# Kernel optimization log

Hardware: AMD Instinct MI355X
Metric: run time of the kernel (lower is better)

## Reference

```python
import jax, jax.numpy as jnp
import numpy as np

N = 262144        # 64^3 grid unknowns
NNZ = 7 * N       # ~7-point stencil sparsity
BS = 32


def setup_inputs() -> dict:
    key = jax.random.key(0)
    k1, k2, k3, k4, k5 = jax.random.split(key, 5)
    y_pred = jax.random.normal(k1, (BS, N), dtype=jnp.float32)
    y_true = jax.random.normal(k2, (BS, N), dtype=jnp.float32)
    A_vals = jax.random.normal(k3, (NNZ,), dtype=jnp.float32)
    A_rows = jax.random.randint(k4, (NNZ,), 0, N, dtype=jnp.int32)
    A_cols = jax.random.randint(k5, (NNZ,), 0, N, dtype=jnp.int32)
    return {"y_pred": y_pred, "y_true": y_true, "A_vals": A_vals,
            "A_rows": A_rows, "A_cols": A_cols}


def reference(y_pred, y_true, A_vals, A_rows, A_cols):
    # YhatY[b] = <y_true[b], y_pred[b]>
    YhatY = jnp.sum(y_true * y_pred, axis=1)                      # (bs,)
    # Sparse matvec per batch: YhatAt = (A @ y_pred.T).T, COO form.
    # gathered[e, b] = A_vals[e] * y_pred[b, A_cols[e]]
    gathered = (y_pred[:, A_cols] * A_vals).T                     # (nnz, bs)
    YhatAt = jax.ops.segment_sum(gathered, A_rows, num_segments=N).T  # (bs, N)
    # YhatYhatAt[b] = <y_pred[b], A y_pred[b]>
    YhatYhatAt = jnp.sum(y_pred * YhatAt, axis=1)                 # (bs,)
    # diag(YhatY / YhatYhatAt) @ YhatAt == row-wise scale by alpha
    alpha = YhatY / YhatYhatAt                                    # (bs,)
    resid = y_true - alpha[:, None] * YhatAt                      # (bs, N)
    return jnp.mean(jnp.sum(resid * resid, axis=1))
```

## Files before the change

### kernel.cpp

```cpp
#include <hip/hip_runtime.h>

#define NGRID 262144
#define NNZ_C 1835008
#define TP    260


__global__ __launch_bounds__(256) void k_prep(
        const float* __restrict__ yp, const float* __restrict__ yt,
        float* __restrict__ yp_t, float* __restrict__ yat_t,
        float* __restrict__ p1) {
    __shared__ __align__(16) float T[32 * TP];
    __shared__ float p1red[32];
    const int tid = threadIdx.x;
    const int l = tid & 63, w = tid >> 6;
    const size_t n0 = (size_t)blockIdx.x * 256;
    #pragma unroll
    for (int s = 0; s < 8; ++s) {
        const int b = s * 4 + w;
        const float4 a = *(const float4*)(yp + (size_t)b * NGRID + n0 + 4 * l);
        const float4 t = *(const float4*)(yt + (size_t)b * NGRID + n0 + 4 * l);
        *(float4*)(&T[b * TP + 4 * l]) = a;
        float sty = a.x * t.x + a.y * t.y + a.z * t.z + a.w * t.w;
        #pragma unroll
        for (int o = 32; o > 0; o >>= 1) sty += __shfl_down(sty, o);
        if (l == 0) p1red[b] = sty;
    }
    __syncthreads();
    float4* ypt4 = (float4*)(yp_t + n0 * 32);
    float4* yat4 = (float4*)(yat_t + n0 * 32);
    #pragma unroll
    for (int q = 0; q < 8; ++q) {
        const int f = q * 256 + tid;
        const int n = f >> 3;
        const int bb = 4 * (f & 7);
        float4 v;
        v.x = T[(bb + 0) * TP + n];
        v.y = T[(bb + 1) * TP + n];
        v.z = T[(bb + 2) * TP + n];
        v.w = T[(bb + 3) * TP + n];
        ypt4[f] = v;
        yat4[f] = make_float4(0.f, 0.f, 0.f, 0.f);
    }
    if (tid < 32) p1[blockIdx.x * 32 + tid] = p1red[tid];
}

__global__ void k_scatter(const float* __restrict__ vals,
                          const int* __restrict__ rows,
                          const int* __restrict__ cols,
                          const float* __restrict__ yp_t,
                          float* __restrict__ yat_t) {
    const size_t tid = (size_t)blockIdx.x * blockDim.x + threadIdx.x;
    const int b = (int)(tid & 31);
    const size_t e = tid >> 5;
    const float v = vals[e];
    const int r = rows[e];
    const int c = cols[e];
    const float x = yp_t[(size_t)c * 32 + b];
    atomicAdd(&yat_t[(size_t)r * 32 + b], v * x);
}

__global__ __launch_bounds__(256) void k_post(
        const float* __restrict__ yat_t, const float* __restrict__ yp_t,
        const float* __restrict__ yt, float* __restrict__ p2) {
    __shared__ float tile[256 * 33];
    __shared__ float red[2][256];
    const int tid = threadIdx.x;
    const size_t n0 = (size_t)blockIdx.x * 256;

    float c1 = 0.f, c3 = 0.f;
    #pragma unroll
    for (int i = 0; i < 32; ++i) {
        const int f = i * 256 + tid;
        const float a = yat_t[n0 * 32 + f];
        const float p = yp_t[n0 * 32 + f];
        c1 = fmaf(p, a, c1);
        c3 = fmaf(a, a, c3);
        tile[(f >> 5) * 33 + (f & 31)] = a;
    }
    red[0][tid] = c1;
    red[1][tid] = c3;
    __syncthreads();

    const int w = tid >> 6;
    const int lane = tid & 63;
    #pragma unroll
    for (int j = 0; j < 8; ++j) {
        const int b = w * 8 + j;
        const float* ytr = yt + (size_t)b * NGRID + n0;
        float c2 = 0.f, tt = 0.f;
        #pragma unroll
        for (int c = 0; c < 4; ++c) {
            const int nl = c * 64 + lane;
            const float t = ytr[nl];
            const float yv = tile[nl * 33 + b];
            c2 = fmaf(t, yv, c2);
            tt = fmaf(t, t, tt);
        }
        #pragma unroll
        for (int o = 32; o > 0; o >>= 1) {
            c2 += __shfl_down(c2, o);
            tt += __shfl_down(tt, o);
        }
        if (lane == 0) {
            p2[blockIdx.x * 128 + 32 + b] = c2;
            p2[blockIdx.x * 128 + 96 + b] = tt;
        }
    }

    if (tid < 32) {
        float s1 = 0.f, s3 = 0.f;
        #pragma unroll
        for (int k = 0; k < 8; ++k) {
            s1 += red[0][tid + 32 * k];
            s3 += red[1][tid + 32 * k];
        }
        p2[blockIdx.x * 128 + 0 + tid] = s1;
        p2[blockIdx.x * 128 + 64 + tid] = s3;
    }
}

__global__ __launch_bounds__(256) void k_finish(
        const float* __restrict__ p2, const float* __restrict__ p1,
        float* __restrict__ out) {
    __shared__ float tot[128];
    __shared__ float styv[32];
    __shared__ float lb[32];
    const int tid = threadIdx.x;
    if (tid < 128) {
        float acc = 0.f;
        for (int j = 0; j < 1024; ++j) acc += p2[(size_t)j * 128 + tid];
        tot[tid] = acc;
    } else if (tid < 160) {
        const int b = tid - 128;
        float acc = 0.f;
        for (int j = 0; j < 1024; ++j) acc += p1[(size_t)j * 32 + b];
        styv[b] = acc;
    }
    __syncthreads();
    if (tid < 32) {
        const float c1 = tot[tid];
        const float c2 = tot[32 + tid];
        const float c3 = tot[64 + tid];
        const float stt = tot[96 + tid];
        const float a = styv[tid] / c1;
        lb[tid] = fmaf(a * a, c3, fmaf(-2.f * a, c2, stt));
    }
    __syncthreads();
    if (tid == 0) {
        float s = 0.f;
        #pragma unroll
        for (int i = 0; i < 32; ++i) s += lb[i];
        out[0] = s * (1.0f / 32.0f);
    }
}

extern "C" void kernel_launch(void* const* d_in, const int* in_sizes, int n_in,
                              void* d_out, int out_size, void* d_ws, size_t ws_size,
                              hipStream_t stream) {
    const float* yp = (const float*)d_in[0];
    const float* yt = (const float*)d_in[1];
    const float* Av = (const float*)d_in[2];
    const int*   Ar = (const int*)d_in[3];
    const int*   Ac = (const int*)d_in[4];
    float* out = (float*)d_out;

    float* ws    = (float*)d_ws;
    float* yp_t  = ws;
    float* yat_t = yp_t + (size_t)NGRID * 32;
    float* p1    = yat_t + (size_t)NGRID * 32;
    float* p2    = p1 + 1024 * 32;

    k_prep<<<NGRID / 256, 256, 0, stream>>>(yp, yt, yp_t, yat_t, p1);
    k_scatter<<<(NNZ_C * 32) / 256, 256, 0, stream>>>(Av, Ar, Ac, yp_t, yat_t);
    k_post<<<NGRID / 256, 256, 0, stream>>>(yat_t, yp_t, yt, p2);
    k_finish<<<1, 256, 0, stream>>>(p2, p1, out);
}
```

Baseline: 348.1 us.

## Transpose y_true in prep and make post reductions fully vectorized

The prep kernel now also transposes y_true into a node-major workspace, so the post kernel reads yat, yp and yt all in the same contiguous float4 layout. The post kernel accumulates all five dot-product partials (including <y_true, y_pred>) in registers, with no shared-memory transpose tile. The final reduction is split into a 64-block stage and a single-block stage instead of one serial block looping over 1024 partials. In exchange there is an extra 32 MB write and read of y_true, and the post grid doubles with 160 partials per block.

```diff
diff --git a/kernel.cpp b/kernel.cpp
--- a/kernel.cpp
+++ b/kernel.cpp
@@ -7,26 +7,22 @@
 
 __global__ __launch_bounds__(256) void k_prep(
         const float* __restrict__ yp, const float* __restrict__ yt,
-        float* __restrict__ yp_t, float* __restrict__ yat_t,
-        float* __restrict__ p1) {
+        float* __restrict__ yp_t, float* __restrict__ yt_t,
+        float* __restrict__ yat_t) {
     __shared__ __align__(16) float T[32 * TP];
-    __shared__ float p1red[32];
     const int tid = threadIdx.x;
     const int l = tid & 63, w = tid >> 6;
-    const size_t n0 = (size_t)blockIdx.x * 256;
+    const int fam = blockIdx.x >> 10;
+    const size_t n0 = (size_t)(blockIdx.x & 1023) * 256;
+    const float* src = fam ? yt : yp;
     #pragma unroll
     for (int s = 0; s < 8; ++s) {
         const int b = s * 4 + w;
-        const float4 a = *(const float4*)(yp + (size_t)b * NGRID + n0 + 4 * l);
-        const float4 t = *(const float4*)(yt + (size_t)b * NGRID + n0 + 4 * l);
+        const float4 a = *(const float4*)(src + (size_t)b * NGRID + n0 + 4 * l);
         *(float4*)(&T[b * TP + 4 * l]) = a;
-        float sty = a.x * t.x + a.y * t.y + a.z * t.z + a.w * t.w;
-        #pragma unroll
-        for (int o = 32; o > 0; o >>= 1) sty += __shfl_down(sty, o);
-        if (l == 0) p1red[b] = sty;
     }
     __syncthreads();
-    float4* ypt4 = (float4*)(yp_t + n0 * 32);
+    float4* dst4 = (float4*)((fam ? yt_t : yp_t) + n0 * 32);
     float4* yat4 = (float4*)(yat_t + n0 * 32);
     #pragma unroll
     for (int q = 0; q < 8; ++q) {
@@ -38,10 +34,9 @@
         v.y = T[(bb + 1) * TP + n];
         v.z = T[(bb + 2) * TP + n];
         v.w = T[(bb + 3) * TP + n];
-        ypt4[f] = v;
-        yat4[f] = make_float4(0.f, 0.f, 0.f, 0.f);
+        dst4[f] = v;
+        if (!fam) yat4[f] = make_float4(0.f, 0.f, 0.f, 0.f);
     }
-    if (tid < 32) p1[blockIdx.x * 32 + tid] = p1red[tid];
 }
 
 __global__ void k_scatter(const float* __restrict__ vals,
@@ -61,88 +56,84 @@
 
 __global__ __launch_bounds__(256) void k_post(
         const float* __restrict__ yat_t, const float* __restrict__ yp_t,
-        const float* __restrict__ yt, float* __restrict__ p2) {
-    __shared__ float tile[256 * 33];
-    __shared__ float red[2][256];
+        const float* __restrict__ yt_t, float* __restrict__ p2) {
+    __shared__ float redA[5][1024];
     const int tid = threadIdx.x;
-    const size_t n0 = (size_t)blockIdx.x * 256;
-
-    float c1 = 0.f, c3 = 0.f;
+    const size_t base = (size_t)blockIdx.x * 1024;
+    const float4* yat4 = (const float4*)yat_t;
+    const float4* yp4 = (const float4*)yp_t;
+    const float4* yt4 = (const float4*)yt_t;
+    float c1[4] = {0,0,0,0}, c2[4] = {0,0,0,0}, c3[4] = {0,0,0,0};
+    float tt[4] = {0,0,0,0}, sy[4] = {0,0,0,0};
     #pragma unroll
-    for (int i = 0; i < 32; ++i) {
-        const int f = i * 256 + tid;
-        const float a = yat_t[n0 * 32 + f];
-        const float p = yp_t[n0 * 32 + f];
-        c1 = fmaf(p, a, c1);
-        c3 = fmaf(a, a, c3);
-        tile[(f >> 5) * 33 + (f & 31)] = a;
+    for (int q = 0; q < 4; ++q) {
+        const size_t f = base + q * 256 + tid;
+        const float4 a = yat4[f];
+        const float4 p = yp4[f];
+        const float4 t = yt4[f];
+        c1[0] = fmaf(p.x, a.x, c1[0]); c2[0] = fmaf(t.x, a.x, c2[0]);
+        c3[0] = fmaf(a.x, a.x, c3[0]); tt[0] = fmaf(t.x, t.x, tt[0]);
+        sy[0] = fmaf(t.x, p.x, sy[0]);
+        c1[1] = fmaf(p.y, a.y, c1[1]); c2[1] = fmaf(t.y, a.y, c2[1]);
+        c3[1] = fmaf(a.y, a.y, c3[1]); tt[1] = fmaf(t.y, t.y, tt[1]);
+        sy[1] = fmaf(t.y, p.y, sy[1]);
+        c1[2] = fmaf(p.z, a.z, c1[2]); c2[2] = fmaf(t.z, a.z, c2[2]);
+        c3[2] = fmaf(a.z, a.z, c3[2]); tt[2] = fmaf(t.z, t.z, tt[2]);
+        sy[2] = fmaf(t.z, p.z, sy[2]);
+        c1[3] = fmaf(p.w, a.w, c1[3]); c2[3] = fmaf(t.w, a.w, c2[3]);
+        c3[3] = fmaf(a.w, a.w, c3[3]); tt[3] = fmaf(t.w, t.w, tt[3]);
+        sy[3] = fmaf(t.w, p.w, sy[3]);
     }
-    red[0][tid] = c1;
-    red[1][tid] = c3;
+    #pragma unroll
+    for (int k = 0; k < 4; ++k) {
+        redA[0][4 * tid + k] = c1[k];
+        redA[1][4 * tid + k] = c2[k];
+        redA[2][4 * tid + k] = c3[k];
+        redA[3][4 * tid + k] = tt[k];
+        redA[4][4 * tid + k] = sy[k];
+    }
     __syncthreads();
-
-    const int w = tid >> 6;
-    const int lane = tid & 63;
-    #pragma unroll
-    for (int j = 0; j < 8; ++j) {
-        const int b = w * 8 + j;
-        const float* ytr = yt + (size_t)b * NGRID + n0;
-        float c2 = 0.f, tt = 0.f;
+    if (tid < 32) {
         #pragma unroll
-        for (int c = 0; c < 4; ++c) {
-            const int nl = c * 64 + lane;
-            const float t = ytr[nl];
-            const float yv = tile[nl * 33 + b];
-            c2 = fmaf(t, yv, c2);
-            tt = fmaf(t, t, tt);
+        for (int s = 0; s < 5; ++s) {
+            float acc = 0.f;
+            #pragma unroll
+            for (int j = 0; j < 32; ++j) acc += redA[s][tid + 32 * j];
+            p2[blockIdx.x * 160 + s * 32 + tid] = acc;
         }
-        #pragma unroll
-        for (int o = 32; o > 0; o >>= 1) {
-            c2 += __shfl_down(c2, o);
-            tt += __shfl_down(tt, o);
-        }
-        if (lane == 0) {
-            p2[blockIdx.x * 128 + 32 + b] = c2;
-            p2[blockIdx.x * 128 + 96 + b] = tt;
-        }
-    }
-
-    if (tid < 32) {
-        float s1 = 0.f, s3 = 0.f;
-        #pragma unroll
-        for (int k = 0; k < 8; ++k) {
-            s1 += red[0][tid + 32 * k];
-            s3 += red[1][tid + 32 * k];
-        }
-        p2[blockIdx.x * 128 + 0 + tid] = s1;
-        p2[blockIdx.x * 128 + 64 + tid] = s3;
     }
 }
 
-__global__ __launch_bounds__(256) void k_finish(
-        const float* __restrict__ p2, const float* __restrict__ p1,
-        float* __restrict__ out) {
-    __shared__ float tot[128];
-    __shared__ float styv[32];
+__global__ __launch_bounds__(256) void k_finish1(
+        const float* __restrict__ p2, float* __restrict__ pr2) {
+    const int tid = threadIdx.x, g = blockIdx.x;
+    if (tid < 160) {
+        float acc = 0.f;
+        #pragma unroll
+        for (int j = 0; j < 32; ++j) acc += p2[(size_t)(g * 32 + j) * 160 + tid];
+        pr2[g * 160 + tid] = acc;
+    }
+}
+
+__global__ __launch_bounds__(256) void k_finish2(
+        const float* __restrict__ pr2, float* __restrict__ out) {
+    __shared__ float tot[160];
     __shared__ float lb[32];
     const int tid = threadIdx.x;
-    if (tid < 128) {
+    if (tid < 160) {
         float acc = 0.f;
-        for (int j = 0; j < 1024; ++j) acc += p2[(size_t)j * 128 + tid];
+        #pragma unroll
+        for (int j = 0; j < 64; ++j) acc += pr2[j * 160 + tid];
         tot[tid] = acc;
-    } else if (tid < 160) {
-        const int b = tid - 128;
-        float acc = 0.f;
-        for (int j = 0; j < 1024; ++j) acc += p1[(size_t)j * 32 + b];
-        styv[b] = acc;
     }
     __syncthreads();
     if (tid < 32) {
-        const float c1 = tot[tid];
+        const float c1 = tot[0 + tid];
         const float c2 = tot[32 + tid];
         const float c3 = tot[64 + tid];
         const float stt = tot[96 + tid];
-        const float a = styv[tid] / c1;
+        const float sty = tot[128 + tid];
+        const float a = sty / c1;
         lb[tid] = fmaf(a * a, c3, fmaf(-2.f * a, c2, stt));
     }
     __syncthreads();
@@ -167,11 +158,13 @@
     float* ws    = (float*)d_ws;
     float* yp_t  = ws;
     float* yat_t = yp_t + (size_t)NGRID * 32;
-    float* p1    = yat_t + (size_t)NGRID * 32;
-    float* p2    = p1 + 1024 * 32;
+    float* yt_t  = yat_t + (size_t)NGRID * 32;
+    float* p2    = yt_t + (size_t)NGRID * 32;
+    float* pr2   = p2 + 2048 * 160;
 
-    k_prep<<<NGRID / 256, 256, 0, stream>>>(yp, yt, yp_t, yat_t, p1);
+    k_prep<<<2048, 256, 0, stream>>>(yp, yt, yp_t, yt_t, yat_t);
     k_scatter<<<(NNZ_C * 32) / 256, 256, 0, stream>>>(Av, Ar, Ac, yp_t, yat_t);
-    k_post<<<NGRID / 256, 256, 0, stream>>>(yat_t, yp_t, yt, p2);
-    k_finish<<<1, 256, 0, stream>>>(p2, p1, out);
+    k_post<<<2048, 256, 0, stream>>>(yat_t, yp_t, yt_t, p2);
+    k_finish1<<<64, 256, 0, stream>>>(p2, pr2);
+    k_finish2<<<1, 256, 0, stream>>>(pr2, out);
 }
```

Result: faster. 330.7 us (-5.0%).
